# Kernel optimization log

Hardware: AMD Instinct MI355X
Metric: run time of the kernel (lower is better)

## Reference

```python
import jax, jax.numpy as jnp
import numpy as np

NU = 8192   # num_users
NI = 8192   # num_items
B = 4096    # batch_size
D = 64      # embed_size
NS = 5      # num_scores


def _w(key, fan_in, fan_out):
    # xavier-uniform-like init
    lim = np.sqrt(6.0 / (fan_in + fan_out)).astype(np.float32)
    return jax.random.uniform(key, (fan_in, fan_out), jnp.float32, -lim, lim)


def setup_inputs() -> dict:
    key = jax.random.key(0)
    ks = jax.random.split(key, 32)
    z = lambda n: jnp.zeros((n,), jnp.float32)
    inp = {
        "batch_user": jax.random.randint(ks[0], (B,), 0, NU),
        "batch_item": jax.random.randint(ks[1], (B,), 0, NI),
        "R": jax.random.uniform(ks[2], (NU, NI), jnp.float32),
        "S": jax.random.uniform(ks[3], (NU, NU), jnp.float32),
        "U": _w(ks[4], NU, D),
        "V": _w(ks[5], NI, D),
        "w_r": _w(ks[6], NS, D), "b_r": z(D),
        "Wu0": _w(ks[7], 2 * D, D), "bu0": z(D), "Wu1": _w(ks[8], D, D), "bu1": z(D),
        "Wv0": _w(ks[9], 2 * D, D), "bv0": z(D), "Wv1": _w(ks[10], D, D), "bv1": z(D),
        "Wc0": _w(ks[11], 2 * D, D), "bc0": z(D), "Wc1": _w(ks[12], D, D), "bc1": z(D),
        "Wg0": _w(ks[13], 2 * D, D), "bg0": z(D), "Wg1": _w(ks[14], D, D), "bg1": z(D),
        "W_I": _w(ks[15], D, D), "b_I": z(D),
        "W_Sm": _w(ks[16], D, D), "b_Sm": z(D),
        "W1A": _w(ks[17], 2 * D, D), "b1A": z(D), "w2A": _w(ks[18], D, 1), "b2A": z(1),
        "W1B": _w(ks[19], 2 * D, D), "b1B": z(D), "w2B": _w(ks[20], D, 1), "b2B": z(1),
        "W1M": _w(ks[21], 2 * D, D), "b1M": z(D), "w2M": _w(ks[22], D, 1), "b2M": z(1),
        "W_Z": _w(ks[23], D, D), "b_Z": z(D),
    }
    return inp


def reference(batch_user, batch_item, R, S, U, V, w_r, b_r,
              Wu0, bu0, Wu1, bu1, Wv0, bv0, Wv1, bv1,
              Wc0, bc0, Wc1, bc1, Wg0, bg0, Wg1, bg1,
              W_I, b_I, W_Sm, b_Sm,
              W1A, b1A, w2A, b2A, W1B, b1B, w2B, b2B,
              W1M, b1M, w2M, b2M, W_Z, b_Z):
    relu = jax.nn.relu
    # rating embedding: e_r = Linear(num_scores->d) applied to vector [1..num_scores]
    e_r = jnp.arange(1, w_r.shape[0] + 1, dtype=w_r.dtype) @ w_r + b_r  # [d]
    Uc = jnp.concatenate([U, jnp.broadcast_to(e_r, U.shape)], axis=1)  # [NU, 2d]
    Vc = jnp.concatenate([V, jnp.broadcast_to(e_r, V.shape)], axis=1)  # [NI, 2d]
    # per-node MLP stacks (num_layer=2; layer0: 2d->d, layer1: d->d)
    Uh = relu(relu(Uc @ Wu0 + bu0) @ Wu1 + bu1)  # [NU, d]
    Vh = relu(relu(Vc @ Wv0 + bv0) @ Wv1 + bv1)  # [NI, d]
    Ub = Uh[batch_user]  # [B, d]
    Vb = Vh[batch_item]  # [B, d]
    # item-space attention A over batch, softmax along batch dim
    A = jax.nn.softmax(relu(jnp.concatenate([Vb, Ub], axis=1) @ W1A + b1A) @ w2A + b2A, axis=0)  # [B,1]
    # attention-weighted sparse-row aggregation over item embeddings
    H_I = relu(((R[batch_user] * A) @ Vh) @ W_I + b_I)  # [B, d]
    Bw = jax.nn.softmax(relu(jnp.concatenate([H_I, Ub], axis=1) @ W1B + b1B) @ w2B + b2B, axis=0)  # [B,1]
    H_S = relu(((S[batch_user] * Bw) @ Uh) @ W_Sm + b_Sm)  # [B, d]
    H = jnp.concatenate([H_I, H_S], axis=1)  # [B, 2d]
    H = relu(relu(H @ Wc0 + bc0) @ Wc1 + bc1)  # [B, d]
    M = jax.nn.softmax(relu(jnp.concatenate([Ub, Vb], axis=1) @ W1M + b1M) @ w2M + b2M, axis=0)  # [B,1]
    # R.T row-gather: columns of R for batch items -> [B, NU]
    Rt_b = jnp.take(R, batch_item, axis=1).T
    Z = relu(((Rt_b * M) @ Uh) @ W_Z + b_Z)  # [B, d]
    G = jnp.concatenate([H, Z], axis=1)  # [B, 2d]
    G = relu(relu(G @ Wg0 + bg0) @ Wg1 + bg1)  # [B, d]
    return G
```

## Files before the change

### kernel.cpp

```cpp
#include <hip/hip_runtime.h>
#include <stdint.h>


typedef short bf16x8 __attribute__((ext_vector_type(8)));
typedef float f32x4 __attribute__((ext_vector_type(4)));

#define PKZ     16
#define PKLEN   512
#define PKITERS 16
#define QKZ     32
#define QKLEN   256
#define QKITERS 8

__device__ __forceinline__ unsigned f2bf1(float f) {
    unsigned x = __float_as_uint(f);
    return (x + 0x7FFFu + ((x >> 16) & 1u)) >> 16;
}

__device__ __forceinline__ float wsum(float v) {
    #pragma unroll
    for (int o = 32; o; o >>= 1) v += __shfl_xor(v, o);
    return v;
}

__device__ __forceinline__ void block_softmax_stats(const float* __restrict__ s,
                                                    float& m, float& inv) {
    __shared__ float r1[4];
    __shared__ float r2[4];
    int t = threadIdx.x, lane = t & 63, wv = t >> 6;
    float lm = -3.4e38f;
    #pragma unroll
    for (int i = 0; i < 16; ++i) lm = fmaxf(lm, s[t + 256 * i]);
    #pragma unroll
    for (int o = 32; o; o >>= 1) lm = fmaxf(lm, __shfl_xor(lm, o));
    if (lane == 0) r1[wv] = lm;
    __syncthreads();
    m = fmaxf(fmaxf(r1[0], r1[1]), fmaxf(r1[2], r1[3]));
    float ls = 0.f;
    #pragma unroll
    for (int i = 0; i < 16; ++i) ls += __expf(s[t + 256 * i] - m);
    ls = wsum(ls);
    if (lane == 0) r2[wv] = ls;
    __syncthreads();
    inv = 1.f / (r2[0] + r2[1] + r2[2] + r2[3]);
}

__global__ __launch_bounds__(256) void k_mlp(
    const float* __restrict__ U, const float* __restrict__ V,
    const float* __restrict__ w_r, const float* __restrict__ b_r,
    const float* __restrict__ Wu0, const float* __restrict__ bu0,
    const float* __restrict__ Wu1, const float* __restrict__ bu1,
    const float* __restrict__ Wv0, const float* __restrict__ bv0,
    const float* __restrict__ Wv1, const float* __restrict__ bv1,
    float* __restrict__ Uh, float* __restrict__ Vh,
    unsigned short* __restrict__ Uhb, unsigned short* __restrict__ Vhb)
{
    int gt = blockIdx.x * 256 + threadIdx.x;
    int wid = gt >> 6;
    int lane = gt & 63;

    float er = b_r[lane];
    #pragma unroll
    for (int s = 0; s < 5; ++s) er += (float)(s + 1) * w_r[s * 64 + lane];

    const int isV = (wid >= 2048);
    const float* X  = isV ? V   : U;
    const float* W0 = isV ? Wv0 : Wu0;
    const float* B0 = isV ? bv0 : bu0;
    const float* W1 = isV ? Wv1 : Wu1;
    const float* B1 = isV ? bv1 : bu1;
    float* Hout          = isV ? Vh  : Uh;
    unsigned short* Hb   = isV ? Vhb : Uhb;
    int r0 = (wid & 2047) * 4;

    float x[4];
    #pragma unroll
    for (int j = 0; j < 4; ++j) x[j] = X[(r0 + j) * 64 + lane];

    float h0c = B0[lane];
    for (int k = 0; k < 64; ++k) h0c += __shfl(er, k) * W0[(64 + k) * 64 + lane];

    float h0[4];
    #pragma unroll
    for (int j = 0; j < 4; ++j) h0[j] = h0c;
    for (int k = 0; k < 64; ++k) {
        float wv = W0[k * 64 + lane];
        #pragma unroll
        for (int j = 0; j < 4; ++j) h0[j] += __shfl(x[j], k) * wv;
    }
    #pragma unroll
    for (int j = 0; j < 4; ++j) h0[j] = fmaxf(h0[j], 0.f);

    float h1[4];
    #pragma unroll
    for (int j = 0; j < 4; ++j) h1[j] = B1[lane];
    for (int k = 0; k < 64; ++k) {
        float wv = W1[k * 64 + lane];
        #pragma unroll
        for (int j = 0; j < 4; ++j) h1[j] += __shfl(h0[j], k) * wv;
    }
    #pragma unroll
    for (int j = 0; j < 4; ++j) {
        h1[j] = fmaxf(h1[j], 0.f);
        Hout[(r0 + j) * 64 + lane] = h1[j];
    }
    unsigned pw[2];
    #pragma unroll
    for (int q = 0; q < 2; ++q) pw[q] = f2bf1(h1[2*q]) | (f2bf1(h1[2*q+1]) << 16);
    unsigned short* dst = Hb + (size_t)(r0 >> 3) * 512 + (lane >> 4) * 128
                        + (lane & 15) * 8 + (r0 & 7);
    *(uint2*)dst = make_uint2(pw[0], pw[1]);
}

__global__ __launch_bounds__(256, 4) void k_gemm(
    const float* __restrict__ R, const float* __restrict__ S,
    const int* __restrict__ bu,
    const unsigned short* __restrict__ Uhb, const unsigned short* __restrict__ Vhb,
    float* __restrict__ PpI, float* __restrict__ PpS, float* __restrict__ Qp)
{
    __shared__ float lds[2][2048];
    const int bid = blockIdx.x;
    const int t = threadIdx.x;
    const int w = t >> 6, l = t & 63, lg = l >> 4, lr = l & 15;

    f32x4 acc[4] = {};

    if (bid < 2 * PKZ * 64) {
        const int gP = PKZ * 64;
        const int isS = bid >= gP;
        int q = isS ? bid - gP : bid;
        int tile = q & 63, kz = q >> 6;
        int brow = tile * 64 + w * 16 + lr;
        int ridx = bu[brow];
        const float* A = (isS ? S : R) + (size_t)ridx * 8192 + kz * PKLEN + lg * 8;
        const unsigned short* Bb = (isS ? Uhb : Vhb)
                                 + (size_t)((kz * PKLEN) >> 3) * 512 + lr * 8;

        f32x4 b0[4], b1[4];
        #pragma unroll
        for (int d = 0; d < 4; ++d) {
            b0[d] = ((const f32x4*)(A + d * 32))[0];
            b1[d] = ((const f32x4*)(A + d * 32))[1];
        }

        #pragma unroll 4
        for (int ks = 0; ks < PKITERS - 4; ++ks) {
            const int slot = ks & 3;
            union { bf16x8 v; unsigned u[4]; } af;
            af.u[0] = f2bf1(b0[slot].x) | (f2bf1(b0[slot].y) << 16);
            af.u[1] = f2bf1(b0[slot].z) | (f2bf1(b0[slot].w) << 16);
            af.u[2] = f2bf1(b1[slot].x) | (f2bf1(b1[slot].y) << 16);
            af.u[3] = f2bf1(b1[slot].z) | (f2bf1(b1[slot].w) << 16);
            b0[slot] = ((const f32x4*)(A + (ks + 4) * 32))[0];
            b1[slot] = ((const f32x4*)(A + (ks + 4) * 32))[1];
            const unsigned short* bp = Bb + (size_t)(ks * 4 + lg) * 512;
            #pragma unroll
            for (int c = 0; c < 4; ++c) {
                bf16x8 bf = *(const bf16x8*)(bp + c * 128);
                acc[c] = __builtin_amdgcn_mfma_f32_16x16x32_bf16(af.v, bf, acc[c], 0, 0, 0);
            }
        }
        #pragma unroll
        for (int ks = PKITERS - 4; ks < PKITERS; ++ks) {
            const int slot = ks & 3;
            union { bf16x8 v; unsigned u[4]; } af;
            af.u[0] = f2bf1(b0[slot].x) | (f2bf1(b0[slot].y) << 16);
            af.u[1] = f2bf1(b0[slot].z) | (f2bf1(b0[slot].w) << 16);
            af.u[2] = f2bf1(b1[slot].x) | (f2bf1(b1[slot].y) << 16);
            af.u[3] = f2bf1(b1[slot].z) | (f2bf1(b1[slot].w) << 16);
            const unsigned short* bp = Bb + (size_t)(ks * 4 + lg) * 512;
            #pragma unroll
            for (int c = 0; c < 4; ++c) {
                bf16x8 bf = *(const bf16x8*)(bp + c * 128);
                acc[c] = __builtin_amdgcn_mfma_f32_16x16x32_bf16(af.v, bf, acc[c], 0, 0, 0);
            }
        }

        float* out = (isS ? PpS : PpI)
                   + (size_t)(kz * 4096 + tile * 64 + w * 16 + lg * 4) * 64 + lr;
        #pragma unroll
        for (int c = 0; c < 4; ++c) {
            #pragma unroll
            for (int j = 0; j < 4; ++j) out[j * 64 + c * 16] = acc[c][j];
        }
    } else {
        int q = bid - 2 * PKZ * 64;
        const int tile = q & 127;
        const int kz   = q >> 7;
        const int i0 = tile * 64;
        const int u0 = kz * QKLEN;

        const float* gbase = R + ((size_t)u0 + (t >> 4)) * 8192 + i0 + (t & 15) * 4;

        #pragma unroll
        for (int qq = 0; qq < 2; ++qq) {
            const float* g = gbase + (size_t)(qq * 16) * 8192;
            __builtin_amdgcn_global_load_lds(
                (const __attribute__((address_space(1))) void*)g,
                (__attribute__((address_space(3))) void*)&lds[0][(qq * 256 + t) * 4],
                16, 0, 0);
        }
        __syncthreads();

        const int iloc = w * 16 + lr;
        for (int s = 0; s < QKITERS; ++s) {
            if (s + 1 < QKITERS) {
                int nb = (s + 1) & 1;
                #pragma unroll
                for (int qq = 0; qq < 2; ++qq) {
                    const float* g = gbase + (size_t)((s + 1) * 32 + qq * 16) * 8192;
                    __builtin_amdgcn_global_load_lds(
                        (const __attribute__((address_space(1))) void*)g,
                        (__attribute__((address_space(3))) void*)&lds[nb][(qq * 256 + t) * 4],
                        16, 0, 0);
                }
            }
            const float* Lb = lds[s & 1];
            float av[8];
            #pragma unroll
            for (int j = 0; j < 8; ++j) av[j] = Lb[(8 * lg + j) * 64 + iloc];
            union { bf16x8 v; unsigned u[4]; } af;
            #pragma unroll
            for (int qq = 0; qq < 4; ++qq)
                af.u[qq] = f2bf1(av[2*qq]) | (f2bf1(av[2*qq+1]) << 16);
            const unsigned short* bp = Uhb + (size_t)((u0 >> 3) + s * 4 + lg) * 512 + lr * 8;
            #pragma unroll
            for (int c = 0; c < 4; ++c) {
                bf16x8 bf = *(const bf16x8*)(bp + c * 128);
                acc[c] = __builtin_amdgcn_mfma_f32_16x16x32_bf16(af.v, bf, acc[c], 0, 0, 0);
            }
            __syncthreads();
        }

        float* out = Qp + (size_t)(kz * 8192 + tile * 64 + w * 16 + lg * 4) * 64 + lr;
        #pragma unroll
        for (int c = 0; c < 4; ++c) {
            #pragma unroll
            for (int j = 0; j < 4; ++j) out[j * 64 + c * 16] = acc[c][j];
        }
    }
}

__global__ __launch_bounds__(256) void k_scoreAM(
    const int* __restrict__ bu, const int* __restrict__ bi,
    const float* __restrict__ Uh, const float* __restrict__ Vh,
    const float* __restrict__ W1A, const float* __restrict__ b1A,
    const float* __restrict__ w2A, const float* __restrict__ b2A,
    const float* __restrict__ W1M, const float* __restrict__ b1M,
    const float* __restrict__ w2M, const float* __restrict__ b2M,
    float* __restrict__ sA, float* __restrict__ sM)
{
    int gt = blockIdx.x * 256 + threadIdx.x;
    int wid = gt >> 6, lane = gt & 63;
    int b0 = wid * 2;
    float ub[2], vb[2];
    #pragma unroll
    for (int j = 0; j < 2; ++j) {
        ub[j] = Uh[(size_t)bu[b0 + j] * 64 + lane];
        vb[j] = Vh[(size_t)bi[b0 + j] * 64 + lane];
    }
    float hA[2], hM[2];
    #pragma unroll
    for (int j = 0; j < 2; ++j) { hA[j] = b1A[lane]; hM[j] = b1M[lane]; }
    for (int k = 0; k < 64; ++k) {
        float wa0 = W1A[k * 64 + lane], wa1 = W1A[(64 + k) * 64 + lane];
        float wm0 = W1M[k * 64 + lane], wm1 = W1M[(64 + k) * 64 + lane];
        #pragma unroll
        for (int j = 0; j < 2; ++j) {
            float sv = __shfl(vb[j], k), su = __shfl(ub[j], k);
            hA[j] += sv * wa0 + su * wa1;
            hM[j] += su * wm0 + sv * wm1;
        }
    }
    float w2a = w2A[lane], w2m = w2M[lane];
    #pragma unroll
    for (int j = 0; j < 2; ++j) {
        float sa = wsum(fmaxf(hA[j], 0.f) * w2a);
        float sm = wsum(fmaxf(hM[j], 0.f) * w2m);
        if (lane == 0) { sA[b0 + j] = sa + b2A[0]; sM[b0 + j] = sm + b2M[0]; }
    }
}

__global__ __launch_bounds__(256) void k_HI_scoreB(
    const float* __restrict__ PpI, const float* __restrict__ sA,
    const int* __restrict__ bu, const float* __restrict__ Uh,
    const float* __restrict__ W_I, const float* __restrict__ b_I,
    const float* __restrict__ W1B, const float* __restrict__ b1B,
    const float* __restrict__ w2B, const float* __restrict__ b2B,
    float* __restrict__ HI, float* __restrict__ sB)
{
    float m, inv;
    block_softmax_stats(sA, m, inv);
    int wid = blockIdx.x * 4 + (threadIdx.x >> 6);
    int lane = threadIdx.x & 63;
    int b0 = wid * 2;
    float p[2];
    #pragma unroll
    for (int j = 0; j < 2; ++j) {
        int b = b0 + j;
        float a = 0.f;
        #pragma unroll 8
        for (int kz = 0; kz < PKZ; ++kz)
            a += PpI[(size_t)(kz * 4096 + b) * 64 + lane];
        p[j] = a * (__expf(sA[b] - m) * inv);
    }
    float h[2];
    #pragma unroll
    for (int j = 0; j < 2; ++j) h[j] = b_I[lane];
    for (int k = 0; k < 64; ++k) {
        float wv = W_I[k * 64 + lane];
        #pragma unroll
        for (int j = 0; j < 2; ++j) h[j] += __shfl(p[j], k) * wv;
    }
    float ub[2];
    #pragma unroll
    for (int j = 0; j < 2; ++j) {
        h[j] = fmaxf(h[j], 0.f);
        HI[(size_t)(b0 + j) * 64 + lane] = h[j];
        ub[j] = Uh[(size_t)bu[b0 + j] * 64 + lane];
    }
    float h2[2];
    #pragma unroll
    for (int j = 0; j < 2; ++j) h2[j] = b1B[lane];
    for (int k = 0; k < 64; ++k) {
        float w0 = W1B[k * 64 + lane], w1 = W1B[(64 + k) * 64 + lane];
        #pragma unroll
        for (int j = 0; j < 2; ++j) h2[j] += __shfl(h[j], k) * w0 + __shfl(ub[j], k) * w1;
    }
    float w2 = w2B[lane];
    #pragma unroll
    for (int j = 0; j < 2; ++j) {
        float sv = wsum(fmaxf(h2[j], 0.f) * w2);
        if (lane == 0) sB[b0 + j] = sv + b2B[0];
    }
}

__global__ __launch_bounds__(256) void k_HS_H(
    const float* __restrict__ PpS, const float* __restrict__ sB,
    const float* __restrict__ HI,
    const float* __restrict__ W_Sm, const float* __restrict__ b_Sm,
    const float* __restrict__ Wc0, const float* __restrict__ bc0,
    const float* __restrict__ Wc1, const float* __restrict__ bc1,
    float* __restrict__ Hout)
{
    float m, inv;
    block_softmax_stats(sB, m, inv);
    int wid = blockIdx.x * 4 + (threadIdx.x >> 6);
    int lane = threadIdx.x & 63;
    int b0 = wid * 2;
    float p[2];
    #pragma unroll
    for (int j = 0; j < 2; ++j) {
        int b = b0 + j;
        float a = 0.f;
        #pragma unroll 8
        for (int kz = 0; kz < PKZ; ++kz)
            a += PpS[(size_t)(kz * 4096 + b) * 64 + lane];
        p[j] = a * (__expf(sB[b] - m) * inv);
    }
    float hs[2];
    #pragma unroll
    for (int j = 0; j < 2; ++j) hs[j] = b_Sm[lane];
    for (int k = 0; k < 64; ++k) {
        float wv = W_Sm[k * 64 + lane];
        #pragma unroll
        for (int j = 0; j < 2; ++j) hs[j] += __shfl(p[j], k) * wv;
    }
    float hi[2];
    #pragma unroll
    for (int j = 0; j < 2; ++j) {
        hs[j] = fmaxf(hs[j], 0.f);
        hi[j] = HI[(size_t)(b0 + j) * 64 + lane];
    }
    float h0[2];
    #pragma unroll
    for (int j = 0; j < 2; ++j) h0[j] = bc0[lane];
    for (int k = 0; k < 64; ++k) {
        float w0 = Wc0[k * 64 + lane], w1 = Wc0[(64 + k) * 64 + lane];
        #pragma unroll
        for (int j = 0; j < 2; ++j) h0[j] += __shfl(hi[j], k) * w0 + __shfl(hs[j], k) * w1;
    }
    #pragma unroll
    for (int j = 0; j < 2; ++j) h0[j] = fmaxf(h0[j], 0.f);
    float h1[2];
    #pragma unroll
    for (int j = 0; j < 2; ++j) h1[j] = bc1[lane];
    for (int k = 0; k < 64; ++k) {
        float wv = Wc1[k * 64 + lane];
        #pragma unroll
        for (int j = 0; j < 2; ++j) h1[j] += __shfl(h0[j], k) * wv;
    }
    #pragma unroll
    for (int j = 0; j < 2; ++j) Hout[(size_t)(b0 + j) * 64 + lane] = fmaxf(h1[j], 0.f);
}

__global__ __launch_bounds__(256) void k_Z_G(
    const float* __restrict__ Qp, const float* __restrict__ sM,
    const int* __restrict__ bi, const float* __restrict__ H,
    const float* __restrict__ W_Z, const float* __restrict__ b_Z,
    const float* __restrict__ Wg0, const float* __restrict__ bg0,
    const float* __restrict__ Wg1, const float* __restrict__ bg1,
    float* __restrict__ G)
{
    float m, inv;
    block_softmax_stats(sM, m, inv);
    int wid = blockIdx.x * 4 + (threadIdx.x >> 6);
    int lane = threadIdx.x & 63;
    int b0 = wid * 2;
    float p[2];
    #pragma unroll
    for (int j = 0; j < 2; ++j) {
        int b = b0 + j;
        int it = bi[b];
        float a = 0.f;
        #pragma unroll 8
        for (int kz = 0; kz < QKZ; ++kz)
            a += Qp[(size_t)(kz * 8192 + it) * 64 + lane];
        p[j] = a * (__expf(sM[b] - m) * inv);
    }
    float z[2];
    #pragma unroll
    for (int j = 0; j < 2; ++j) z[j] = b_Z[lane];
    for (int k = 0; k < 64; ++k) {
        float wv = W_Z[k * 64 + lane];
        #pragma unroll
        for (int j = 0; j < 2; ++j) z[j] += __shfl(p[j], k) * wv;
    }
    float hr[2];
    #pragma unroll
    for (int j = 0; j < 2; ++j) {
        z[j] = fmaxf(z[j], 0.f);
        hr[j] = H[(size_t)(b0 + j) * 64 + lane];
    }
    float g0[2];
    #pragma unroll
    for (int j = 0; j < 2; ++j) g0[j] = bg0[lane];
    for (int k = 0; k < 64; ++k) {
        float w0 = Wg0[k * 64 + lane], w1 = Wg0[(64 + k) * 64 + lane];
        #pragma unroll
        for (int j = 0; j < 2; ++j) g0[j] += __shfl(hr[j], k) * w0 + __shfl(z[j], k) * w1;
    }
    #pragma unroll
    for (int j = 0; j < 2; ++j) g0[j] = fmaxf(g0[j], 0.f);
    float g1[2];
    #pragma unroll
    for (int j = 0; j < 2; ++j) g1[j] = bg1[lane];
    for (int k = 0; k < 64; ++k) {
        float wv = Wg1[k * 64 + lane];
        #pragma unroll
        for (int j = 0; j < 2; ++j) g1[j] += __shfl(g0[j], k) * wv;
    }
    #pragma unroll
    for (int j = 0; j < 2; ++j) G[(size_t)(b0 + j) * 64 + lane] = fmaxf(g1[j], 0.f);
}

extern "C" void kernel_launch(void* const* d_in, const int* in_sizes, int n_in,
                              void* d_out, int out_size, void* d_ws, size_t ws_size,
                              hipStream_t stream)
{
    (void)in_sizes; (void)n_in; (void)out_size; (void)ws_size;
    const int*   bu  = (const int*)  d_in[0];
    const int*   bi  = (const int*)  d_in[1];
    const float* R   = (const float*)d_in[2];
    const float* S   = (const float*)d_in[3];
    const float* U   = (const float*)d_in[4];
    const float* V   = (const float*)d_in[5];
    const float* w_r = (const float*)d_in[6];
    const float* b_r = (const float*)d_in[7];
    const float* Wu0 = (const float*)d_in[8];
    const float* bu0 = (const float*)d_in[9];
    const float* Wu1 = (const float*)d_in[10];
    const float* bu1 = (const float*)d_in[11];
    const float* Wv0 = (const float*)d_in[12];
    const float* bv0 = (const float*)d_in[13];
    const float* Wv1 = (const float*)d_in[14];
    const float* bv1 = (const float*)d_in[15];
    const float* Wc0 = (const float*)d_in[16];
    const float* bc0 = (const float*)d_in[17];
    const float* Wc1 = (const float*)d_in[18];
    const float* bc1 = (const float*)d_in[19];
    const float* Wg0 = (const float*)d_in[20];
    const float* bg0 = (const float*)d_in[21];
    const float* Wg1 = (const float*)d_in[22];
    const float* bg1 = (const float*)d_in[23];
    const float* W_I = (const float*)d_in[24];
    const float* b_I = (const float*)d_in[25];
    const float* W_Sm= (const float*)d_in[26];
    const float* b_Sm= (const float*)d_in[27];
    const float* W1A = (const float*)d_in[28];
    const float* b1A = (const float*)d_in[29];
    const float* w2A = (const float*)d_in[30];
    const float* b2A = (const float*)d_in[31];
    const float* W1B = (const float*)d_in[32];
    const float* b1B = (const float*)d_in[33];
    const float* w2B = (const float*)d_in[34];
    const float* b2B = (const float*)d_in[35];
    const float* W1M = (const float*)d_in[36];
    const float* b1M = (const float*)d_in[37];
    const float* w2M = (const float*)d_in[38];
    const float* b2M = (const float*)d_in[39];
    const float* W_Z = (const float*)d_in[40];
    const float* b_Z = (const float*)d_in[41];

    char* ws = (char*)d_ws;
    size_t off = 0;
    float*          Uh  = (float*)(ws + off);          off += 2ull << 20;
    float*          Vh  = (float*)(ws + off);          off += 2ull << 20;
    unsigned short* Uhb = (unsigned short*)(ws + off); off += 1ull << 20;
    unsigned short* Vhb = (unsigned short*)(ws + off); off += 1ull << 20;
    float*          PpI = (float*)(ws + off);          off += (size_t)PKZ << 20;
    float*          PpS = (float*)(ws + off);          off += (size_t)PKZ << 20;
    float*          Qp  = (float*)(ws + off);          off += (size_t)(2 * QKZ) << 20;
    float*          sA  = (float*)(ws + off);
    float*          sM  = sA + 4096;
    float*          sB  = sA + 8192;                   off += 3 * 4096 * 4 + 4096;
    float*          HI  = (float*)(ws + off);          off += 1ull << 20;
    float*          Hh  = (float*)(ws + off);

    k_mlp<<<1024, 256, 0, stream>>>(U, V, w_r, b_r, Wu0, bu0, Wu1, bu1,
                                    Wv0, bv0, Wv1, bv1, Uh, Vh, Uhb, Vhb);
    k_gemm<<<2 * PKZ * 64 + 128 * QKZ, 256, 0, stream>>>(R, S, bu, Uhb, Vhb,
                                                         PpI, PpS, Qp);
    k_scoreAM<<<512, 256, 0, stream>>>(bu, bi, Uh, Vh, W1A, b1A, w2A, b2A,
                                       W1M, b1M, w2M, b2M, sA, sM);
    k_HI_scoreB<<<512, 256, 0, stream>>>(PpI, sA, bu, Uh, W_I, b_I,
                                         W1B, b1B, w2B, b2B, HI, sB);
    k_HS_H<<<512, 256, 0, stream>>>(PpS, sB, HI, W_Sm, b_Sm, Wc0, bc0, Wc1, bc1,
                                    Hh);
    k_Z_G<<<512, 256, 0, stream>>>(Qp, sM, bi, Hh, W_Z, b_Z, Wg0, bg0, Wg1, bg1,
                                   (float*)d_out);
}
```

Baseline: 235.3 us.

## Stage embedding B-tiles in LDS and double split-K count for P GEMMs

Each k_gemm block now copies its whole bf16 Uh/Vh K-slice into shared memory with global_load_lds, instead of every wave reading B fragments straight from global memory. This applies to both the P (R/S row-gather) path and the Q (R transpose) path. The P path's split-K goes from 16 to 32, which halves K per block and makes a single fully unrolled loop. Launch bounds drop to 3 blocks per CU to fit the larger LDS footprint. The aim is to cut redundant global/L2 B traffic and raise parallelism, at the cost of twice as many P partial sums to write and reduce, plus lower occupancy.

Measured after the change: 246.1 us. 1.05x slower.

```diff
diff --git a/kernel.cpp b/kernel.cpp
--- a/kernel.cpp
+++ b/kernel.cpp
@@ -5,12 +5,13 @@
 typedef short bf16x8 __attribute__((ext_vector_type(8)));
 typedef float f32x4 __attribute__((ext_vector_type(4)));
 
-#define PKZ     16
-#define PKLEN   512
-#define PKITERS 16
-#define QKZ     32
-#define QKLEN   256
-#define QKITERS 8
+#define PKZ      32
+#define PKLEN    256
+#define PKITERS  8
+#define QKZ      32
+#define QKLEN    256
+#define QKITERS  8
+#define P_BLOCKS (2 * PKZ * 64)
 
 __device__ __forceinline__ unsigned f2bf1(float f) {
     unsigned x = __float_as_uint(f);
@@ -112,29 +113,38 @@
     *(uint2*)dst = make_uint2(pw[0], pw[1]);
 }
 
-__global__ __launch_bounds__(256, 4) void k_gemm(
+__global__ __launch_bounds__(256, 3) void k_gemm(
     const float* __restrict__ R, const float* __restrict__ S,
     const int* __restrict__ bu,
     const unsigned short* __restrict__ Uhb, const unsigned short* __restrict__ Vhb,
     float* __restrict__ PpI, float* __restrict__ PpS, float* __restrict__ Qp)
 {
-    __shared__ float lds[2][2048];
+    __shared__ short Bsl[16384];
+    __shared__ float Abuf[2][2048];
     const int bid = blockIdx.x;
     const int t = threadIdx.x;
     const int w = t >> 6, l = t & 63, lg = l >> 4, lr = l & 15;
 
     f32x4 acc[4] = {};
 
-    if (bid < 2 * PKZ * 64) {
+    if (bid < P_BLOCKS) {
         const int gP = PKZ * 64;
         const int isS = bid >= gP;
         int q = isS ? bid - gP : bid;
         int tile = q & 63, kz = q >> 6;
+
+        const char* Bg = (const char*)((isS ? Uhb : Vhb) + (size_t)kz * 16384);
+        #pragma unroll
+        for (int ii = 0; ii < 8; ++ii) {
+            __builtin_amdgcn_global_load_lds(
+                (const __attribute__((address_space(1))) void*)(Bg + ii * 4096 + t * 16),
+                (__attribute__((address_space(3))) void*)((char*)Bsl + ii * 4096 + t * 16),
+                16, 0, 0);
+        }
+
         int brow = tile * 64 + w * 16 + lr;
         int ridx = bu[brow];
         const float* A = (isS ? S : R) + (size_t)ridx * 8192 + kz * PKLEN + lg * 8;
-        const unsigned short* Bb = (isS ? Uhb : Vhb)
-                                 + (size_t)((kz * PKLEN) >> 3) * 512 + lr * 8;
 
         f32x4 b0[4], b1[4];
         #pragma unroll
@@ -142,39 +152,27 @@
             b0[d] = ((const f32x4*)(A + d * 32))[0];
             b1[d] = ((const f32x4*)(A + d * 32))[1];
         }
-
-        #pragma unroll 4
-        for (int ks = 0; ks < PKITERS - 4; ++ks) {
+        __syncthreads();
+
+        #pragma unroll
+        for (int ks = 0; ks < PKITERS; ++ks) {
             const int slot = ks & 3;
             union { bf16x8 v; unsigned u[4]; } af;
             af.u[0] = f2bf1(b0[slot].x) | (f2bf1(b0[slot].y) << 16);
             af.u[1] = f2bf1(b0[slot].z) | (f2bf1(b0[slot].w) << 16);
             af.u[2] = f2bf1(b1[slot].x) | (f2bf1(b1[slot].y) << 16);
             af.u[3] = f2bf1(b1[slot].z) | (f2bf1(b1[slot].w) << 16);
-            b0[slot] = ((const f32x4*)(A + (ks + 4) * 32))[0];
-            b1[slot] = ((const f32x4*)(A + (ks + 4) * 32))[1];
-            const unsigned short* bp = Bb + (size_t)(ks * 4 + lg) * 512;
+            if (ks + 4 < PKITERS) {
+                b0[slot] = ((const f32x4*)(A + (ks + 4) * 32))[0];
+                b1[slot] = ((const f32x4*)(A + (ks + 4) * 32))[1];
+            }
+            const short* bp = Bsl + (ks * 4 + lg) * 512 + lr * 8;
             #pragma unroll
             for (int c = 0; c < 4; ++c) {
                 bf16x8 bf = *(const bf16x8*)(bp + c * 128);
                 acc[c] = __builtin_amdgcn_mfma_f32_16x16x32_bf16(af.v, bf, acc[c], 0, 0, 0);
             }
         }
-        #pragma unroll
-        for (int ks = PKITERS - 4; ks < PKITERS; ++ks) {
-            const int slot = ks & 3;
-            union { bf16x8 v; unsigned u[4]; } af;
-            af.u[0] = f2bf1(b0[slot].x) | (f2bf1(b0[slot].y) << 16);
-            af.u[1] = f2bf1(b0[slot].z) | (f2bf1(b0[slot].w) << 16);
-            af.u[2] = f2bf1(b1[slot].x) | (f2bf1(b1[slot].y) << 16);
-            af.u[3] = f2bf1(b1[slot].z) | (f2bf1(b1[slot].w) << 16);
-            const unsigned short* bp = Bb + (size_t)(ks * 4 + lg) * 512;
-            #pragma unroll
-            for (int c = 0; c < 4; ++c) {
-                bf16x8 bf = *(const bf16x8*)(bp + c * 128);
-                acc[c] = __builtin_amdgcn_mfma_f32_16x16x32_bf16(af.v, bf, acc[c], 0, 0, 0);
-            }
-        }
 
         float* out = (isS ? PpS : PpI)
                    + (size_t)(kz * 4096 + tile * 64 + w * 16 + lg * 4) * 64 + lr;
@@ -184,20 +182,28 @@
             for (int j = 0; j < 4; ++j) out[j * 64 + c * 16] = acc[c][j];
         }
     } else {
-        int q = bid - 2 * PKZ * 64;
+        int q = bid - P_BLOCKS;
         const int tile = q & 127;
         const int kz   = q >> 7;
         const int i0 = tile * 64;
         const int u0 = kz * QKLEN;
 
+        const char* Bg = (const char*)(Uhb + (size_t)kz * 16384);
+        #pragma unroll
+        for (int ii = 0; ii < 8; ++ii) {
+            __builtin_amdgcn_global_load_lds(
+                (const __attribute__((address_space(1))) void*)(Bg + ii * 4096 + t * 16),
+                (__attribute__((address_space(3))) void*)((char*)Bsl + ii * 4096 + t * 16),
+                16, 0, 0);
+        }
+
         const float* gbase = R + ((size_t)u0 + (t >> 4)) * 8192 + i0 + (t & 15) * 4;
-
         #pragma unroll
         for (int qq = 0; qq < 2; ++qq) {
             const float* g = gbase + (size_t)(qq * 16) * 8192;
             __builtin_amdgcn_global_load_lds(
                 (const __attribute__((address_space(1))) void*)g,
-                (__attribute__((address_space(3))) void*)&lds[0][(qq * 256 + t) * 4],
+                (__attribute__((address_space(3))) void*)&Abuf[0][(qq * 256 + t) * 4],
                 16, 0, 0);
         }
         __syncthreads();
@@ -211,11 +217,11 @@
                     const float* g = gbase + (size_t)((s + 1) * 32 + qq * 16) * 8192;
                     __builtin_amdgcn_global_load_lds(
                         (const __attribute__((address_space(1))) void*)g,
-                        (__attribute__((address_space(3))) void*)&lds[nb][(qq * 256 + t) * 4],
+                        (__attribute__((address_space(3))) void*)&Abuf[nb][(qq * 256 + t) * 4],
                         16, 0, 0);
                 }
             }
-            const float* Lb = lds[s & 1];
+            const float* Lb = Abuf[s & 1];
             float av[8];
             #pragma unroll
             for (int j = 0; j < 8; ++j) av[j] = Lb[(8 * lg + j) * 64 + iloc];
@@ -223,7 +229,7 @@
             #pragma unroll
             for (int qq = 0; qq < 4; ++qq)
                 af.u[qq] = f2bf1(av[2*qq]) | (f2bf1(av[2*qq+1]) << 16);
-            const unsigned short* bp = Uhb + (size_t)((u0 >> 3) + s * 4 + lg) * 512 + lr * 8;
+            const short* bp = Bsl + (s * 4 + lg) * 512 + lr * 8;
             #pragma unroll
             for (int c = 0; c < 4; ++c) {
                 bf16x8 bf = *(const bf16x8*)(bp + c * 128);
@@ -519,8 +525,8 @@
 
     k_mlp<<<1024, 256, 0, stream>>>(U, V, w_r, b_r, Wu0, bu0, Wu1, bu1,
                                     Wv0, bv0, Wv1, bv1, Uh, Vh, Uhb, Vhb);
-    k_gemm<<<2 * PKZ * 64 + 128 * QKZ, 256, 0, stream>>>(R, S, bu, Uhb, Vhb,
-                                                         PpI, PpS, Qp);
+    k_gemm<<<P_BLOCKS + 128 * QKZ, 256, 0, stream>>>(R, S, bu, Uhb, Vhb,
+                                                     PpI, PpS, Qp);
     k_scoreAM<<<512, 256, 0, stream>>>(bu, bi, Uh, Vh, W1A, b1A, w2A, b2A,
                                        W1M, b1M, w2M, b2M, sA, sM);
     k_HI_scoreB<<<512, 256, 0, stream>>>(PpI, sA, bu, Uh, W_I, b_I,
```

## Restructure fused GEMM: triple-buffered LDS Q tiles, fewer K splits, interleaved block roles

Applied to the files above, without the earlier changes.

The Q path (R^T @ Uh over the whole user dimension) now uses wider 128-column tiles with 1024-row K slabs. Both the R tile and the Uh bf16 fragments are staged into LDS through a three-deep async global_load_lds pipeline, with explicit vmcnt waits and barriers. The P path halves its split-K count (8 splits of 1024), and Q and P blocks are interleaved one-in-three in the grid so the two workloads share the GPU. The aim is fewer partial-sum writes and re-reads and better latency hiding on the large streaming reads of R. The cost is about 60KB of LDS per block, which lowers occupancy, and the hand-written waitcnt counts are fragile.

After: 201.3 us. 1.17x faster.

```diff
diff --git a/kernel.cpp b/kernel.cpp
--- a/kernel.cpp
+++ b/kernel.cpp
@@ -5,12 +5,15 @@
 typedef short bf16x8 __attribute__((ext_vector_type(8)));
 typedef float f32x4 __attribute__((ext_vector_type(4)));
 
-#define PKZ     16
-#define PKLEN   512
-#define PKITERS 16
-#define QKZ     32
-#define QKLEN   256
-#define QKITERS 8
+#define PKZ      8
+#define PKLEN    1024
+#define PKITERS  32
+#define QKZ      8
+#define QSLAB    1024
+#define QW       128
+#define QSTEPS   32
+#define QBLOCKS  512
+#define PBLOCKS  1024
 
 __device__ __forceinline__ unsigned f2bf1(float f) {
     unsigned x = __float_as_uint(f);
@@ -112,30 +115,115 @@
     *(uint2*)dst = make_uint2(pw[0], pw[1]);
 }
 
-__global__ __launch_bounds__(256, 4) void k_gemm(
+__global__ __launch_bounds__(256) void k_gemm(
     const float* __restrict__ R, const float* __restrict__ S,
     const int* __restrict__ bu,
     const unsigned short* __restrict__ Uhb, const unsigned short* __restrict__ Vhb,
     float* __restrict__ PpI, float* __restrict__ PpS, float* __restrict__ Qp)
 {
-    __shared__ float lds[2][2048];
+    __shared__ alignas(16) char QLDS[3][20480];
     const int bid = blockIdx.x;
     const int t = threadIdx.x;
     const int w = t >> 6, l = t & 63, lg = l >> 4, lr = l & 15;
 
-    f32x4 acc[4] = {};
-
-    if (bid < 2 * PKZ * 64) {
+    if (bid % 3 == 0) {
+        const int qidx = bid / 3;
+        const int iw = qidx & 63;
+        const int kz = qidx >> 6;
+        const int i0 = iw * QW;
+        const int u0 = kz * QSLAB;
+
+        f32x4 acc[2][4] = {};
+
+        #define QSTAGE(s)                                                         \
+        {                                                                         \
+            char* dstA = QLDS[(s) % 3];                                           \
+            _Pragma("unroll")                                                     \
+            for (int q = 0; q < 4; ++q) {                                         \
+                const int rloc = 2 * (4 * q + w);                                 \
+                const float* g = R + ((size_t)(u0 + (s) * 32 + rloc) + (l >> 5)) * 8192 \
+                               + i0 + (l & 31) * 4;                               \
+                __builtin_amdgcn_global_load_lds(                                 \
+                    (const __attribute__((address_space(1))) void*)g,             \
+                    (__attribute__((address_space(3))) void*)(dstA + rloc * 512 + l * 16), \
+                    16, 0, 0);                                                    \
+            }                                                                     \
+            const char* bsrc = (const char*)Uhb                                   \
+                + ((size_t)((u0 + (s) * 32) >> 3)) * 1024 + w * 1024 + l * 16;    \
+            __builtin_amdgcn_global_load_lds(                                     \
+                (const __attribute__((address_space(1))) void*)bsrc,              \
+                (__attribute__((address_space(3))) void*)(dstA + 16384 + w * 1024 + l * 16), \
+                16, 0, 0);                                                        \
+        }
+
+        #define QCOMP(s)                                                          \
+        {                                                                         \
+            const char* buf = QLDS[(s) % 3];                                      \
+            const float* La = (const float*)buf;                                  \
+            const short* Lbb = (const short*)(buf + 16384);                       \
+            bf16x8 bfrag[4];                                                      \
+            _Pragma("unroll")                                                     \
+            for (int c = 0; c < 4; ++c)                                           \
+                bfrag[c] = *(const bf16x8*)(Lbb + lg * 512 + c * 128 + lr * 8);   \
+            _Pragma("unroll")                                                     \
+            for (int f = 0; f < 2; ++f) {                                         \
+                const int iloc = w * 32 + f * 16 + lr;                            \
+                float av[8];                                                      \
+                _Pragma("unroll")                                                 \
+                for (int j = 0; j < 8; ++j) av[j] = La[(8 * lg + j) * QW + iloc]; \
+                union { bf16x8 v; unsigned u[4]; } af;                            \
+                _Pragma("unroll")                                                 \
+                for (int qq = 0; qq < 4; ++qq)                                    \
+                    af.u[qq] = f2bf1(av[2*qq]) | (f2bf1(av[2*qq+1]) << 16);       \
+                _Pragma("unroll")                                                 \
+                for (int c = 0; c < 4; ++c)                                       \
+                    acc[f][c] = __builtin_amdgcn_mfma_f32_16x16x32_bf16(af.v, bfrag[c], acc[f][c], 0, 0, 0); \
+            }                                                                     \
+        }
+
+        QSTAGE(0); QSTAGE(1); QSTAGE(2);
+
+        for (int s = 0; s < QSTEPS - 2; ++s) {
+            asm volatile("s_waitcnt vmcnt(10)" ::: "memory");
+            __builtin_amdgcn_s_barrier();
+            QCOMP(s);
+            asm volatile("s_waitcnt lgkmcnt(0)" ::: "memory");
+            __builtin_amdgcn_sched_barrier(0);
+            __builtin_amdgcn_s_barrier();
+            if (s + 3 < QSTEPS) QSTAGE(s + 3);
+        }
+        asm volatile("s_waitcnt vmcnt(5)" ::: "memory");
+        __builtin_amdgcn_s_barrier();
+        QCOMP(QSTEPS - 2);
+        asm volatile("s_waitcnt vmcnt(0)" ::: "memory");
+        __builtin_amdgcn_s_barrier();
+        QCOMP(QSTEPS - 1);
+
+        #pragma unroll
+        for (int f = 0; f < 2; ++f) {
+            float* out = Qp + (size_t)(kz * 8192 + i0 + w * 32 + f * 16 + lg * 4) * 64 + lr;
+            #pragma unroll
+            for (int c = 0; c < 4; ++c) {
+                #pragma unroll
+                for (int j = 0; j < 4; ++j) out[j * 64 + c * 16] = acc[f][c][j];
+            }
+        }
+        #undef QSTAGE
+        #undef QCOMP
+    } else {
+        const int pidx = bid - bid / 3 - 1;
         const int gP = PKZ * 64;
-        const int isS = bid >= gP;
-        int q = isS ? bid - gP : bid;
+        const int isS = pidx >= gP;
+        int q = isS ? pidx - gP : pidx;
         int tile = q & 63, kz = q >> 6;
+
         int brow = tile * 64 + w * 16 + lr;
         int ridx = bu[brow];
         const float* A = (isS ? S : R) + (size_t)ridx * 8192 + kz * PKLEN + lg * 8;
         const unsigned short* Bb = (isS ? Uhb : Vhb)
                                  + (size_t)((kz * PKLEN) >> 3) * 512 + lr * 8;
 
+        f32x4 acc[4] = {};
         f32x4 b0[4], b1[4];
         #pragma unroll
         for (int d = 0; d < 4; ++d) {
@@ -183,61 +271,6 @@
             #pragma unroll
             for (int j = 0; j < 4; ++j) out[j * 64 + c * 16] = acc[c][j];
         }
-    } else {
-        int q = bid - 2 * PKZ * 64;
-        const int tile = q & 127;
-        const int kz   = q >> 7;
-        const int i0 = tile * 64;
-        const int u0 = kz * QKLEN;
-
-        const float* gbase = R + ((size_t)u0 + (t >> 4)) * 8192 + i0 + (t & 15) * 4;
-
-        #pragma unroll
-        for (int qq = 0; qq < 2; ++qq) {
-            const float* g = gbase + (size_t)(qq * 16) * 8192;
-            __builtin_amdgcn_global_load_lds(
-                (const __attribute__((address_space(1))) void*)g,
-                (__attribute__((address_space(3))) void*)&lds[0][(qq * 256 + t) * 4],
-                16, 0, 0);
-        }
-        __syncthreads();
-
-        const int iloc = w * 16 + lr;
-        for (int s = 0; s < QKITERS; ++s) {
-            if (s + 1 < QKITERS) {
-                int nb = (s + 1) & 1;
-                #pragma unroll
-                for (int qq = 0; qq < 2; ++qq) {
-                    const float* g = gbase + (size_t)((s + 1) * 32 + qq * 16) * 8192;
-                    __builtin_amdgcn_global_load_lds(
-                        (const __attribute__((address_space(1))) void*)g,
-                        (__attribute__((address_space(3))) void*)&lds[nb][(qq * 256 + t) * 4],
-                        16, 0, 0);
-                }
-            }
-            const float* Lb = lds[s & 1];
-            float av[8];
-            #pragma unroll
-            for (int j = 0; j < 8; ++j) av[j] = Lb[(8 * lg + j) * 64 + iloc];
-            union { bf16x8 v; unsigned u[4]; } af;
-            #pragma unroll
-            for (int qq = 0; qq < 4; ++qq)
-                af.u[qq] = f2bf1(av[2*qq]) | (f2bf1(av[2*qq+1]) << 16);
-            const unsigned short* bp = Uhb + (size_t)((u0 >> 3) + s * 4 + lg) * 512 + lr * 8;
-            #pragma unroll
-            for (int c = 0; c < 4; ++c) {
-                bf16x8 bf = *(const bf16x8*)(bp + c * 128);
-                acc[c] = __builtin_amdgcn_mfma_f32_16x16x32_bf16(af.v, bf, acc[c], 0, 0, 0);
-            }
-            __syncthreads();
-        }
-
-        float* out = Qp + (size_t)(kz * 8192 + tile * 64 + w * 16 + lg * 4) * 64 + lr;
-        #pragma unroll
-        for (int c = 0; c < 4; ++c) {
-            #pragma unroll
-            for (int j = 0; j < 4; ++j) out[j * 64 + c * 16] = acc[c][j];
-        }
     }
 }
 
@@ -299,7 +332,7 @@
     for (int j = 0; j < 2; ++j) {
         int b = b0 + j;
         float a = 0.f;
-        #pragma unroll 8
+        #pragma unroll
         for (int kz = 0; kz < PKZ; ++kz)
             a += PpI[(size_t)(kz * 4096 + b) * 64 + lane];
         p[j] = a * (__expf(sA[b] - m) * inv);
@@ -353,7 +386,7 @@
     for (int j = 0; j < 2; ++j) {
         int b = b0 + j;
         float a = 0.f;
-        #pragma unroll 8
+        #pragma unroll
         for (int kz = 0; kz < PKZ; ++kz)
             a += PpS[(size_t)(kz * 4096 + b) * 64 + lane];
         p[j] = a * (__expf(sB[b] - m) * inv);
@@ -413,7 +446,7 @@
         int b = b0 + j;
         int it = bi[b];
         float a = 0.f;
-        #pragma unroll 8
+        #pragma unroll
         for (int kz = 0; kz < QKZ; ++kz)
             a += Qp[(size_t)(kz * 8192 + it) * 64 + lane];
         p[j] = a * (__expf(sM[b] - m) * inv);
@@ -519,8 +552,8 @@
 
     k_mlp<<<1024, 256, 0, stream>>>(U, V, w_r, b_r, Wu0, bu0, Wu1, bu1,
                                     Wv0, bv0, Wv1, bv1, Uh, Vh, Uhb, Vhb);
-    k_gemm<<<2 * PKZ * 64 + 128 * QKZ, 256, 0, stream>>>(R, S, bu, Uhb, Vhb,
-                                                         PpI, PpS, Qp);
+    k_gemm<<<QBLOCKS + PBLOCKS, 256, 0, stream>>>(R, S, bu, Uhb, Vhb,
+                                                  PpI, PpS, Qp);
     k_scoreAM<<<512, 256, 0, stream>>>(bu, bi, Uh, Vh, W1A, b1A, w2A, b2A,
                                        W1M, b1M, w2M, b2M, sA, sM);
     k_HI_scoreB<<<512, 256, 0, stream>>>(PpI, sA, bu, Uh, W_I, b_I,
```
